# Kernel optimization log

Measured on AMD Instinct MI355X. Metric: run time of the kernel, lower is better.

The kernel has to match this reference:

```python
import jax, jax.numpy as jnp
import numpy as np

SIGMA_P = 0.01  # sigma_p from __init__
T = 2_000_000   # number of time samples / PMD steps


def _pauli():
    # Pauli spin matrices used by Czegledi (2016) rotation model
    return jnp.array([[[1, 0], [0, -1]],
                      [[0, 1], [1, 0]],
                      [[0, -1j], [1j, 0]]], dtype=jnp.complex64)


def setup_inputs() -> dict:
    key = jax.random.key(0)
    k1, k2, k3, k4 = jax.random.split(key, 4)
    signal_re = jax.random.normal(k1, (T, 2), dtype=jnp.float32)
    signal_im = jax.random.normal(k2, (T, 2), dtype=jnp.float32)
    alphas = jax.random.normal(k3, (T, 3), dtype=jnp.float32)  # raw N(0,1); scaled by SIGMA_P inside reference
    # initial Jones matrix J_k1 built from a random unit 4-vector (as in __init__)
    g = jax.random.normal(k4, (4,), dtype=jnp.float32)
    a0 = g / jnp.linalg.norm(g)
    theta0 = jnp.arccos(a0[0])
    alpha = a0[1:] / jnp.sin(theta0) * theta0
    theta = jnp.linalg.norm(alpha)
    a = (alpha / theta).astype(jnp.complex64)
    J0 = (jnp.eye(2, dtype=jnp.complex64) * jnp.cos(theta)
          - 1j * jnp.einsum('a,aij->ij', a, _pauli()) * jnp.sin(theta))
    return {"signal_re": signal_re, "signal_im": signal_im, "alphas": alphas,
            "J0_re": jnp.real(J0), "J0_im": jnp.imag(J0)}


def reference(signal_re, signal_im, alphas, J0_re, J0_im):
    pauli = _pauli()
    al = alphas * SIGMA_P                      # [T,3] per-step rotation vectors
    thetas = jnp.linalg.norm(al, axis=1)       # [T]
    a = (al / thetas[:, None]).astype(jnp.complex64)   # [T,3] unit axes
    eye = jnp.eye(2, dtype=jnp.complex64)
    # per-step incremental Jones matrices: J_delta[k] = I*cos(th) - i*(a.sigma)*sin(th)
    J_delta = (eye[None, :, :] * jnp.cos(thetas)[:, None, None]
               - 1j * jnp.einsum('ka,aij->kij', a, pauli) * jnp.sin(thetas)[:, None, None])  # [T,2,2]
    # cumulative left-product: chain[k] = J_delta[k] @ ... @ J_delta[0]
    chain = jax.lax.associative_scan(lambda x, y: jnp.matmul(y, x), J_delta)  # [T,2,2]
    J0 = (J0_re + 1j * J0_im).astype(jnp.complex64)
    J_k = jnp.einsum('kij,jl->kil', chain, J0)  # [T,2,2] time-varying Jones matrices
    signal = (signal_re + 1j * signal_im).astype(jnp.complex64)  # [T,2]
    return jnp.einsum('kij,kj->ki', J_k, signal)  # [T,2] complex64
```

## Files before the change

kernel.cpp:

```cpp
#include <hip/hip_runtime.h>
#include <hip/hip_bf16.h>

#define BLK 256
#define CH 8

__device__ __forceinline__ float4 qmul(const float4 A, const float4 B) {
    return make_float4(
        A.x*B.x - A.y*B.y - A.z*B.z - A.w*B.w,
        A.x*B.y + B.x*A.y + A.z*B.w - A.w*B.z,
        A.x*B.z + B.x*A.z + A.w*B.y - A.y*B.w,
        A.x*B.w + B.x*A.w + A.y*B.z - A.z*B.y);
}

__device__ __forceinline__ float4 qid() { return make_float4(1.f, 0.f, 0.f, 0.f); }

__device__ __forceinline__ float4 qnorm(const float4 q) {
    float n = rsqrtf(q.x*q.x + q.y*q.y + q.z*q.z + q.w*q.w);
    return make_float4(q.x*n, q.y*n, q.z*n, q.w*n);
}

__device__ __forceinline__ float4 dquat(float a0, float a1, float a2) {
    float x = a0 * 0.01f, y = a1 * 0.01f, z = a2 * 0.01f;
    float t2 = x*x + y*y + z*z;
    float c = 1.f - t2 * (0.5f - t2 * (1.f / 24.f));
    float f = 1.f - t2 * ((1.f / 6.f) - t2 * (1.f / 120.f));
    return make_float4(c, f*x, f*y, f*z);
}

__device__ __forceinline__ float4 qapply(const float4 m, float s0r, float s1r,
                                         float s0i, float s1i) {
    float w = m.x, v1 = m.y, v2 = m.z, v3 = m.w;
    return make_float4(
        w*s0r + v1*s0i - v3*s1r + v2*s1i,
        w*s0i - v1*s0r - v2*s1r - v3*s1i,
        v3*s0r + v2*s0i + w*s1r - v1*s1i,
        v3*s0i - v2*s0r + w*s1i + v1*s1r);
}

__device__ __forceinline__ float4 shfl_up4(const float4 v, int s) {
    return make_float4(__shfl_up(v.x, s), __shfl_up(v.y, s),
                       __shfl_up(v.z, s), __shfl_up(v.w, s));
}
__device__ __forceinline__ float4 shfl_down4(const float4 v, int s) {
    return make_float4(__shfl_down(v.x, s), __shfl_down(v.y, s),
                       __shfl_down(v.z, s), __shfl_down(v.w, s));
}

__device__ __forceinline__ float4 wave_prod_desc(float4 c) {
    #pragma unroll
    for (int s = 1; s < 64; s <<= 1) {
        float4 u = shfl_down4(c, s);
        c = qmul(u, c);
    }
    return c;
}

__device__ __forceinline__ float4 wave_scan_incl(float4 v, int lane) {
    #pragma unroll
    for (int s = 1; s < 64; s <<= 1) {
        float4 u = shfl_up4(v, s);
        if (lane >= s) v = qmul(v, u);
    }
    return v;
}

__device__ __forceinline__ float4 chunk_quats(const float* __restrict__ al,
                                              long long t, long long T,
                                              long long nchunk, float4* d, bool& full) {
    float4 q = qid();
    full = false;
    if (t >= nchunk) {
        #pragma unroll
        for (int j = 0; j < CH; ++j) d[j] = qid();
        return q;
    }
    if ((t + 1) * CH <= T) {
        full = true;
        const float4* ap = reinterpret_cast<const float4*>(al) + (size_t)t * 6;
        float4 v0 = ap[0], v1 = ap[1], v2 = ap[2];
        float4 v3 = ap[3], v4 = ap[4], v5 = ap[5];
        d[0] = dquat(v0.x, v0.y, v0.z);
        d[1] = dquat(v0.w, v1.x, v1.y);
        d[2] = dquat(v1.z, v1.w, v2.x);
        d[3] = dquat(v2.y, v2.z, v2.w);
        d[4] = dquat(v3.x, v3.y, v3.z);
        d[5] = dquat(v3.w, v4.x, v4.y);
        d[6] = dquat(v4.z, v4.w, v5.x);
        d[7] = dquat(v5.y, v5.z, v5.w);
    } else {
        #pragma unroll
        for (int j = 0; j < CH; ++j) {
            long long k = t * CH + j;
            d[j] = (k < T) ? dquat(al[k*3], al[k*3+1], al[k*3+2]) : qid();
        }
    }
    #pragma unroll
    for (int j = 0; j < CH; ++j) q = qmul(d[j], q);
    return qnorm(q);
}

__device__ __forceinline__ float4 chunk_prod(const float* __restrict__ al,
                                             long long t, long long T,
                                             long long nchunk) {
    float4 d[CH];
    bool full;
    return chunk_quats(al, t, T, nchunk, d, full);
}

__device__ __forceinline__ void apply_and_store(
    const float4* d, float4 run, bool full, long long t, long long T,
    const float* __restrict__ sre, const float* __restrict__ sim,
    float* __restrict__ outf) {
    if (full) {
        const float4* rp = reinterpret_cast<const float4*>(sre) + (size_t)t * 4;
        const float4* ip = reinterpret_cast<const float4*>(sim) + (size_t)t * 4;
        float4* op = reinterpret_cast<float4*>(outf) + (size_t)t * 4;
        float4 r0 = rp[0], r1 = rp[1], r2 = rp[2], r3 = rp[3];
        float4 i0 = ip[0], i1 = ip[1], i2 = ip[2], i3 = ip[3];
        float4 p0, p1;
        run = qmul(d[0], run); p0 = qapply(run, r0.x, r0.y, i0.x, i0.y);
        run = qmul(d[1], run); p1 = qapply(run, r0.z, r0.w, i0.z, i0.w);
        op[0] = make_float4(p0.x, p0.z, p1.x, p1.z);
        run = qmul(d[2], run); p0 = qapply(run, r1.x, r1.y, i1.x, i1.y);
        run = qmul(d[3], run); p1 = qapply(run, r1.z, r1.w, i1.z, i1.w);
        op[1] = make_float4(p0.x, p0.z, p1.x, p1.z);
        run = qmul(d[4], run); p0 = qapply(run, r2.x, r2.y, i2.x, i2.y);
        run = qmul(d[5], run); p1 = qapply(run, r2.z, r2.w, i2.z, i2.w);
        op[2] = make_float4(p0.x, p0.z, p1.x, p1.z);
        run = qmul(d[6], run); p0 = qapply(run, r3.x, r3.y, i3.x, i3.y);
        run = qmul(d[7], run); p1 = qapply(run, r3.z, r3.w, i3.z, i3.w);
        op[3] = make_float4(p0.x, p0.z, p1.x, p1.z);
    } else {
        float2* op2 = reinterpret_cast<float2*>(outf);
        #pragma unroll
        for (int j = 0; j < CH; ++j) {
            long long k = t * CH + j;
            if (k < T) {
                run = qmul(d[j], run);
                float4 p = qapply(run, sre[k*2], sre[k*2+1], sim[k*2], sim[k*2+1]);
                op2[k] = make_float2(p.x, p.z);
            }
        }
    }
}

__global__ void __launch_bounds__(BLK) pmd_k1(
    const float* __restrict__ al, float4* __restrict__ A,
    long long T, long long nchunk) {
    __shared__ float4 sW[BLK / 64];
    const int tid = threadIdx.x, lane = tid & 63, wid = tid >> 6;
    const long long t = (long long)blockIdx.x * BLK + tid;
    float4 q = chunk_prod(al, t, T, nchunk);
    float4 wp = wave_prod_desc(q);
    if (lane == 0) sW[wid] = wp;
    __syncthreads();
    if (tid == 0) {
        float4 a = qmul(sW[1], sW[0]);
        a = qmul(sW[2], a);
        a = qmul(sW[3], a);
        A[blockIdx.x] = qnorm(a);
    }
}

template<int EPT>
__global__ void __launch_bounds__(BLK) pmd_k2(
    const float4* __restrict__ A, float4* __restrict__ EB,
    const float* __restrict__ j0re, const float* __restrict__ j0im, int nblk) {
    __shared__ float4 sW[BLK / 64];
    const int tid = threadIdx.x, lane = tid & 63, wid = tid >> 6;
    const int t0 = tid * EPT;
    float4 excl[EPT];
    float4 run = qid();
    #pragma unroll
    for (int e = 0; e < EPT; ++e) {
        excl[e] = run;
        if (t0 + e < nblk) run = qmul(A[t0 + e], run);
    }
    float4 v = wave_scan_incl(run, lane);
    if (lane == 63) sW[wid] = v;
    __syncthreads();
    float4 P = qid();
    for (int w = 0; w < wid; ++w) P = qmul(sW[w], P);
    float4 vprev = shfl_up4(v, 1);
    float4 texcl = (lane == 0) ? P : qmul(vprev, P);
    float4 q0 = make_float4(j0re[0], -j0im[0], -j0im[1], -j0re[1]);
    float4 base = qmul(texcl, q0);
    #pragma unroll
    for (int e = 0; e < EPT; ++e) {
        if (t0 + e < nblk) EB[t0 + e] = qnorm(qmul(excl[e], base));
    }
}

__global__ void __launch_bounds__(BLK) pmd_k3(
    const float* __restrict__ al, const float* __restrict__ sre,
    const float* __restrict__ sim, const float4* __restrict__ EB,
    float* __restrict__ outf, long long T, long long nchunk) {
    __shared__ float4 sW[BLK / 64];
    const int tid = threadIdx.x, lane = tid & 63, wid = tid >> 6;
    const int b = blockIdx.x;
    const long long t = (long long)b * BLK + tid;

    float4 d[CH];
    bool full;
    float4 q = chunk_quats(al, t, T, nchunk, d, full);
    float4 v = wave_scan_incl(q, lane);
    if (lane == 63) sW[wid] = v;
    __syncthreads();
    float4 P = qid();
    for (int w = 0; w < wid; ++w) P = qmul(sW[w], P);
    float4 vprev = shfl_up4(v, 1);
    float4 Xv = (lane == 0) ? P : qmul(vprev, P);
    float4 run = qmul(Xv, EB[b]);
    if (t < nchunk)
        apply_and_store(d, run, full, t, T, sre, sim, outf);
}

__global__ void __launch_bounds__(BLK) pmd_mono(
    const float* __restrict__ al, const float* __restrict__ sre,
    const float* __restrict__ sim, const float* __restrict__ j0re,
    const float* __restrict__ j0im, float* __restrict__ outf, long long T) {
    __shared__ float4 sW[BLK / 64];
    __shared__ float4 sbase;
    const int tid = threadIdx.x, lane = tid & 63, wid = tid >> 6;
    if (tid == 0)
        sbase = make_float4(j0re[0], -j0im[0], -j0im[1], -j0re[1]);
    __syncthreads();
    const long long nchunk = (T + CH - 1) / CH;
    for (long long c0 = 0; c0 < nchunk; c0 += BLK) {
        const long long t = c0 + tid;
        float4 d[CH];
        bool full;
        float4 q = chunk_quats(al, t, T, nchunk, d, full);
        float4 v = wave_scan_incl(q, lane);
        if (lane == 63) sW[wid] = v;
        __syncthreads();
        float4 P = qid();
        for (int w = 0; w < wid; ++w) P = qmul(sW[w], P);
        float4 vprev = shfl_up4(v, 1);
        float4 Xv = (lane == 0) ? P : qmul(vprev, P);
        float4 base = sbase;
        __syncthreads();
        if (tid == BLK - 1) sbase = qnorm(qmul(qmul(v, P), base));
        if (t < nchunk) {
            float4 run = qmul(Xv, base);
            apply_and_store(d, run, full, t, T, sre, sim, outf);
        }
        __syncthreads();
    }
}

extern "C" void kernel_launch(void* const* d_in, const int* in_sizes, int n_in,
                              void* d_out, int out_size, void* d_ws, size_t ws_size,
                              hipStream_t stream) {
    const float* sre  = (const float*)d_in[0];
    const float* sim  = (const float*)d_in[1];
    const float* al   = (const float*)d_in[2];
    const float* j0re = (const float*)d_in[3];
    const float* j0im = (const float*)d_in[4];
    float* outf = (float*)d_out;
    long long T = (long long)in_sizes[2] / 3;
    if (T <= 0) return;

    long long nchunk = (T + CH - 1) / CH;
    long long nblkLL = (nchunk + BLK - 1) / BLK;
    size_t need = (size_t)(2 * nblkLL) * sizeof(float4);

    if (ws_size >= need && nblkLL <= (long long)BLK * 16) {
        int nblk = (int)nblkLL;
        float4* A  = (float4*)d_ws;
        float4* EB = A + nblk;
        pmd_k1<<<nblk, BLK, 0, stream>>>(al, A, T, nchunk);
        if      (nblk <= BLK)      pmd_k2<1> <<<1, BLK, 0, stream>>>(A, EB, j0re, j0im, nblk);
        else if (nblk <= 2 * BLK)  pmd_k2<2> <<<1, BLK, 0, stream>>>(A, EB, j0re, j0im, nblk);
        else if (nblk <= 4 * BLK)  pmd_k2<4> <<<1, BLK, 0, stream>>>(A, EB, j0re, j0im, nblk);
        else if (nblk <= 8 * BLK)  pmd_k2<8> <<<1, BLK, 0, stream>>>(A, EB, j0re, j0im, nblk);
        else                       pmd_k2<16><<<1, BLK, 0, stream>>>(A, EB, j0re, j0im, nblk);
        pmd_k3<<<nblk, BLK, 0, stream>>>(al, sre, sim, EB, outf, T, nchunk);
    } else {
        pmd_mono<<<1, BLK, 0, stream>>>(al, sre, sim, j0re, j0im, outf, T);
    }
}
```

Baseline: 28.88 us.

## Fuse block-reduce and block-prefix kernels using last-block ticket pattern

Merges the per-block quaternion reduction and the single-block prefix scan into one kernel. Each block increments an atomic ticket, and the last block to finish loads all block products into shared memory and computes the exclusive prefixes. The intent is to remove one kernel launch and its dependency gap. In exchange it adds a memset before the launch and a 16KB shared array per block, which may reduce occupancy, and the tail work runs on a single block.

```diff
diff --git a/kernel.cpp b/kernel.cpp
--- a/kernel.cpp
+++ b/kernel.cpp
@@ -3,6 +3,7 @@
 
 #define BLK 256
 #define CH 8
+#define MAXBLK 1024
 
 __device__ __forceinline__ float4 qmul(const float4 A, const float4 B) {
     return make_float4(
@@ -144,12 +145,16 @@
     }
 }
 
-__global__ void __launch_bounds__(BLK) pmd_k1(
-    const float* __restrict__ al, float4* __restrict__ A,
-    long long T, long long nchunk) {
-    __shared__ float4 sW[BLK / 64];
+__global__ void __launch_bounds__(BLK) pmd_k12(
+    const float* __restrict__ al, float4* __restrict__ A, float4* __restrict__ EB,
+    const float* __restrict__ j0re, const float* __restrict__ j0im,
+    unsigned* __restrict__ ticket, long long T, long long nchunk, int nblk) {
+    __shared__ float4 sW[BLK / 64];
+    __shared__ float4 sA[MAXBLK];
+    __shared__ int sIsLast;
     const int tid = threadIdx.x, lane = tid & 63, wid = tid >> 6;
     const long long t = (long long)blockIdx.x * BLK + tid;
+
     float4 q = chunk_prod(al, t, T, nchunk);
     float4 wp = wave_prod_desc(q);
     if (lane == 0) sW[wid] = wp;
@@ -159,23 +164,22 @@
         a = qmul(sW[2], a);
         a = qmul(sW[3], a);
         A[blockIdx.x] = qnorm(a);
-    }
-}
-
-template<int EPT>
-__global__ void __launch_bounds__(BLK) pmd_k2(
-    const float4* __restrict__ A, float4* __restrict__ EB,
-    const float* __restrict__ j0re, const float* __restrict__ j0im, int nblk) {
-    __shared__ float4 sW[BLK / 64];
-    const int tid = threadIdx.x, lane = tid & 63, wid = tid >> 6;
-    const int t0 = tid * EPT;
-    float4 excl[EPT];
+        __threadfence();
+        unsigned old = atomicAdd(ticket, 1u);
+        sIsLast = (old == (unsigned)(nblk - 1));
+    }
+    __syncthreads();
+    if (!sIsLast) return;
+
+    __threadfence();
+    for (int i = tid; i < nblk; i += BLK) sA[i] = A[i];
+    __syncthreads();
+
+    const int ept = (nblk + BLK - 1) / BLK;
+    const int t0 = tid * ept;
     float4 run = qid();
-    #pragma unroll
-    for (int e = 0; e < EPT; ++e) {
-        excl[e] = run;
-        if (t0 + e < nblk) run = qmul(A[t0 + e], run);
-    }
+    for (int e = 0; e < ept; ++e)
+        if (t0 + e < nblk) run = qmul(sA[t0 + e], run);
     float4 v = wave_scan_incl(run, lane);
     if (lane == 63) sW[wid] = v;
     __syncthreads();
@@ -185,9 +189,12 @@
     float4 texcl = (lane == 0) ? P : qmul(vprev, P);
     float4 q0 = make_float4(j0re[0], -j0im[0], -j0im[1], -j0re[1]);
     float4 base = qmul(texcl, q0);
-    #pragma unroll
-    for (int e = 0; e < EPT; ++e) {
-        if (t0 + e < nblk) EB[t0 + e] = qnorm(qmul(excl[e], base));
+    float4 excl = qid();
+    for (int e = 0; e < ept; ++e) {
+        if (t0 + e < nblk) {
+            EB[t0 + e] = qnorm(qmul(excl, base));
+            excl = qmul(sA[t0 + e], excl);
+        }
     }
 }
 
@@ -213,6 +220,53 @@
     float4 run = qmul(Xv, EB[b]);
     if (t < nchunk)
         apply_and_store(d, run, full, t, T, sre, sim, outf);
+}
+
+__global__ void __launch_bounds__(BLK) pmd_k1(
+    const float* __restrict__ al, float4* __restrict__ A,
+    long long T, long long nchunk) {
+    __shared__ float4 sW[BLK / 64];
+    const int tid = threadIdx.x, lane = tid & 63, wid = tid >> 6;
+    const long long t = (long long)blockIdx.x * BLK + tid;
+    float4 q = chunk_prod(al, t, T, nchunk);
+    float4 wp = wave_prod_desc(q);
+    if (lane == 0) sW[wid] = wp;
+    __syncthreads();
+    if (tid == 0) {
+        float4 a = qmul(sW[1], sW[0]);
+        a = qmul(sW[2], a);
+        a = qmul(sW[3], a);
+        A[blockIdx.x] = qnorm(a);
+    }
+}
+
+template<int EPT>
+__global__ void __launch_bounds__(BLK) pmd_k2(
+    const float4* __restrict__ A, float4* __restrict__ EB,
+    const float* __restrict__ j0re, const float* __restrict__ j0im, int nblk) {
+    __shared__ float4 sW[BLK / 64];
+    const int tid = threadIdx.x, lane = tid & 63, wid = tid >> 6;
+    const int t0 = tid * EPT;
+    float4 excl[EPT];
+    float4 run = qid();
+    #pragma unroll
+    for (int e = 0; e < EPT; ++e) {
+        excl[e] = run;
+        if (t0 + e < nblk) run = qmul(A[t0 + e], run);
+    }
+    float4 v = wave_scan_incl(run, lane);
+    if (lane == 63) sW[wid] = v;
+    __syncthreads();
+    float4 P = qid();
+    for (int w = 0; w < wid; ++w) P = qmul(sW[w], P);
+    float4 vprev = shfl_up4(v, 1);
+    float4 texcl = (lane == 0) ? P : qmul(vprev, P);
+    float4 q0 = make_float4(j0re[0], -j0im[0], -j0im[1], -j0re[1]);
+    float4 base = qmul(texcl, q0);
+    #pragma unroll
+    for (int e = 0; e < EPT; ++e) {
+        if (t0 + e < nblk) EB[t0 + e] = qnorm(qmul(excl[e], base));
+    }
 }
 
 __global__ void __launch_bounds__(BLK) pmd_mono(
@@ -263,18 +317,23 @@
 
     long long nchunk = (T + CH - 1) / CH;
     long long nblkLL = (nchunk + BLK - 1) / BLK;
-    size_t need = (size_t)(2 * nblkLL) * sizeof(float4);
+    size_t need = (size_t)(2 * nblkLL) * sizeof(float4) + 4;
 
     if (ws_size >= need && nblkLL <= (long long)BLK * 16) {
         int nblk = (int)nblkLL;
         float4* A  = (float4*)d_ws;
         float4* EB = A + nblk;
-        pmd_k1<<<nblk, BLK, 0, stream>>>(al, A, T, nchunk);
-        if      (nblk <= BLK)      pmd_k2<1> <<<1, BLK, 0, stream>>>(A, EB, j0re, j0im, nblk);
-        else if (nblk <= 2 * BLK)  pmd_k2<2> <<<1, BLK, 0, stream>>>(A, EB, j0re, j0im, nblk);
-        else if (nblk <= 4 * BLK)  pmd_k2<4> <<<1, BLK, 0, stream>>>(A, EB, j0re, j0im, nblk);
-        else if (nblk <= 8 * BLK)  pmd_k2<8> <<<1, BLK, 0, stream>>>(A, EB, j0re, j0im, nblk);
-        else                       pmd_k2<16><<<1, BLK, 0, stream>>>(A, EB, j0re, j0im, nblk);
+        unsigned* ticket = (unsigned*)(EB + nblk);
+        if (nblk <= MAXBLK) {
+            hipMemsetAsync(ticket, 0, sizeof(unsigned), stream);
+            pmd_k12<<<nblk, BLK, 0, stream>>>(al, A, EB, j0re, j0im, ticket,
+                                              T, nchunk, nblk);
+        } else {
+            pmd_k1<<<nblk, BLK, 0, stream>>>(al, A, T, nchunk);
+            if      (nblk <= 4 * BLK)  pmd_k2<4> <<<1, BLK, 0, stream>>>(A, EB, j0re, j0im, nblk);
+            else if (nblk <= 8 * BLK)  pmd_k2<8> <<<1, BLK, 0, stream>>>(A, EB, j0re, j0im, nblk);
+            else                       pmd_k2<16><<<1, BLK, 0, stream>>>(A, EB, j0re, j0im, nblk);
+        }
         pmd_k3<<<nblk, BLK, 0, stream>>>(al, sre, sim, EB, outf, T, nchunk);
     } else {
         pmd_mono<<<1, BLK, 0, stream>>>(al, sre, sim, j0re, j0im, outf, T);
```

Measured after the change: 52.09 us. 80.4% more time.

## Drop middle scan kernel; compute block prefixes via superblock aggregates in consumer

Applied to the files above, without the earlier changes.

Replaces the three-kernel reduce/scan/apply pipeline with two kernels. The first kernel computes per-block quaternion products plus a product per superblock of four blocks. The apply kernel has its first wave reduce all earlier superblock aggregates and then the within-superblock block products to form its exclusive prefix. This removes one kernel launch and the single-block serial scan, but every block now redundantly reads and reduces up to ~1000 superblock aggregates, and the first kernel has fewer, longer-running blocks.

```diff
diff --git a/kernel.cpp b/kernel.cpp
--- a/kernel.cpp
+++ b/kernel.cpp
@@ -3,6 +3,7 @@
 
 #define BLK 256
 #define CH 8
+#define SUPER 4
 
 __device__ __forceinline__ float4 qmul(const float4 A, const float4 B) {
     return make_float4(
@@ -144,6 +145,88 @@
     }
 }
 
+__global__ void __launch_bounds__(BLK) pmd_k1h(
+    const float* __restrict__ al, float4* __restrict__ A, float4* __restrict__ A2,
+    long long T, long long nchunk) {
+    __shared__ float4 sW[SUPER][BLK / 64];
+    const int tid = threadIdx.x, lane = tid & 63, wid = tid >> 6;
+    const int sb = blockIdx.x;
+    #pragma unroll
+    for (int j = 0; j < SUPER; ++j) {
+        long long t = ((long long)sb * SUPER + j) * BLK + tid;
+        float4 q = chunk_prod(al, t, T, nchunk);
+        float4 wp = wave_prod_desc(q);
+        if (lane == 0) sW[j][wid] = wp;
+    }
+    __syncthreads();
+    if (tid == 0) {
+        float4 acc = qid();
+        #pragma unroll
+        for (int j = 0; j < SUPER; ++j) {
+            float4 af = qmul(sW[j][1], sW[j][0]);
+            af = qmul(sW[j][2], af);
+            af = qmul(sW[j][3], af);
+            af = qnorm(af);
+            A[sb * SUPER + j] = af;
+            acc = qmul(af, acc);
+        }
+        A2[sb] = qnorm(acc);
+    }
+}
+
+__global__ void __launch_bounds__(BLK) pmd_k3h(
+    const float* __restrict__ al, const float* __restrict__ sre,
+    const float* __restrict__ sim, const float4* __restrict__ A,
+    const float4* __restrict__ A2, const float* __restrict__ j0re,
+    const float* __restrict__ j0im, float* __restrict__ outf,
+    long long T, long long nchunk) {
+    __shared__ float4 sW[BLK / 64];
+    __shared__ float4 sexcl;
+    const int tid = threadIdx.x, lane = tid & 63, wid = tid >> 6;
+    const int b = blockIdx.x;
+    const long long t = (long long)b * BLK + tid;
+
+    float4 d[CH];
+    bool full;
+    float4 q = chunk_quats(al, t, T, nchunk, d, full);
+    float4 v = wave_scan_incl(q, lane);
+    if (lane == 63) sW[wid] = v;
+
+    if (tid < 64) {
+        const int s = b / SUPER, r = b % SUPER;
+        float4 sp = qid();
+        if (s > 0) {
+            int top = s - 1;
+            int base = (top >> 6) << 6;
+            for (;;) {
+                int j = base + lane;
+                float4 c = (j <= top) ? A2[j] : qid();
+                float4 wp = wave_prod_desc(c);
+                sp = qmul(sp, wp);
+                if (base == 0) break;
+                top = base - 1;
+                base -= 64;
+            }
+        }
+        if (lane == 0) {
+            float4 fine = qid();
+            for (int i = 0; i < r; ++i) fine = qmul(A[s * SUPER + i], fine);
+            float4 tot = qmul(fine, sp);
+            float4 q0 = make_float4(j0re[0], -j0im[0], -j0im[1], -j0re[1]);
+            sexcl = qnorm(qmul(tot, q0));
+        }
+    }
+    __syncthreads();
+
+    float4 P = qid();
+    for (int w = 0; w < wid; ++w) P = qmul(sW[w], P);
+    float4 vprev = shfl_up4(v, 1);
+    float4 Xv = (lane == 0) ? P : qmul(vprev, P);
+    float4 run = qmul(Xv, sexcl);
+    if (t < nchunk)
+        apply_and_store(d, run, full, t, T, sre, sim, outf);
+}
+
 __global__ void __launch_bounds__(BLK) pmd_k1(
     const float* __restrict__ al, float4* __restrict__ A,
     long long T, long long nchunk) {
@@ -199,7 +282,6 @@
     const int tid = threadIdx.x, lane = tid & 63, wid = tid >> 6;
     const int b = blockIdx.x;
     const long long t = (long long)b * BLK + tid;
-
     float4 d[CH];
     bool full;
     float4 q = chunk_quats(al, t, T, nchunk, d, full);
@@ -263,9 +345,18 @@
 
     long long nchunk = (T + CH - 1) / CH;
     long long nblkLL = (nchunk + BLK - 1) / BLK;
-    size_t need = (size_t)(2 * nblkLL) * sizeof(float4);
-
-    if (ws_size >= need && nblkLL <= (long long)BLK * 16) {
+    long long nsupLL = (nblkLL + SUPER - 1) / SUPER;
+    size_t need_h = (size_t)(nsupLL * SUPER + nsupLL) * sizeof(float4);
+    size_t need_f = (size_t)(2 * nblkLL) * sizeof(float4);
+
+    if (ws_size >= need_h && nsupLL <= 1024) {
+        int nblk = (int)nblkLL, nsup = (int)nsupLL;
+        float4* A  = (float4*)d_ws;
+        float4* A2 = A + (size_t)nsup * SUPER;
+        pmd_k1h<<<nsup, BLK, 0, stream>>>(al, A, A2, T, nchunk);
+        pmd_k3h<<<nblk, BLK, 0, stream>>>(al, sre, sim, A, A2, j0re, j0im,
+                                          outf, T, nchunk);
+    } else if (ws_size >= need_f && nblkLL <= (long long)BLK * 16) {
         int nblk = (int)nblkLL;
         float4* A  = (float4*)d_ws;
         float4* EB = A + nblk;
```

Measured after the change: 30.82 us. +6.7%, slower.

## Drop single-block block-scan kernel; each block reduces its own prefix of block aggregates

Applied to the files above, without the earlier changes.

Removes the middle single-workgroup scan kernel that turned per-block quaternion aggregates into exclusive prefixes. Each block of the final kernel now reduces all preceding block aggregates itself, split across its four waves with wave-level products, then combines them with J0. This saves one kernel launch and a serialized single-block step, at the cost of redundant prefix work that grows with block index. With about 977 blocks, each wave reads at most roughly four 64-entry segments.

```diff
diff --git a/kernel.cpp b/kernel.cpp
--- a/kernel.cpp
+++ b/kernel.cpp
@@ -162,43 +162,31 @@
     }
 }
 
-template<int EPT>
-__global__ void __launch_bounds__(BLK) pmd_k2(
-    const float4* __restrict__ A, float4* __restrict__ EB,
-    const float* __restrict__ j0re, const float* __restrict__ j0im, int nblk) {
-    __shared__ float4 sW[BLK / 64];
-    const int tid = threadIdx.x, lane = tid & 63, wid = tid >> 6;
-    const int t0 = tid * EPT;
-    float4 excl[EPT];
-    float4 run = qid();
-    #pragma unroll
-    for (int e = 0; e < EPT; ++e) {
-        excl[e] = run;
-        if (t0 + e < nblk) run = qmul(A[t0 + e], run);
-    }
-    float4 v = wave_scan_incl(run, lane);
-    if (lane == 63) sW[wid] = v;
-    __syncthreads();
-    float4 P = qid();
-    for (int w = 0; w < wid; ++w) P = qmul(sW[w], P);
-    float4 vprev = shfl_up4(v, 1);
-    float4 texcl = (lane == 0) ? P : qmul(vprev, P);
-    float4 q0 = make_float4(j0re[0], -j0im[0], -j0im[1], -j0re[1]);
-    float4 base = qmul(texcl, q0);
-    #pragma unroll
-    for (int e = 0; e < EPT; ++e) {
-        if (t0 + e < nblk) EB[t0 + e] = qnorm(qmul(excl[e], base));
-    }
-}
-
-__global__ void __launch_bounds__(BLK) pmd_k3(
+__global__ void __launch_bounds__(BLK) pmd_k3s(
     const float* __restrict__ al, const float* __restrict__ sre,
-    const float* __restrict__ sim, const float4* __restrict__ EB,
+    const float* __restrict__ sim, const float4* __restrict__ A,
+    const float* __restrict__ j0re, const float* __restrict__ j0im,
     float* __restrict__ outf, long long T, long long nchunk) {
     __shared__ float4 sW[BLK / 64];
+    __shared__ float4 sSp[BLK / 64];
     const int tid = threadIdx.x, lane = tid & 63, wid = tid >> 6;
     const int b = blockIdx.x;
     const long long t = (long long)b * BLK + tid;
+
+    float4 part = qid();
+    if (b > 0) {
+        const int S = ((b - 1) >> 6) + 1;
+        const int R = (S + 3) >> 2;
+        const int s_lo = wid * R;
+        const int s_hi = min(S, s_lo + R);
+        for (int s = s_lo; s < s_hi; ++s) {
+            int idx = (s << 6) + lane;
+            float4 c = (idx <= b - 1) ? A[idx] : qid();
+            float4 sp = wave_prod_desc(c);
+            part = qmul(sp, part);
+        }
+    }
+    if (lane == 0) sSp[wid] = part;
 
     float4 d[CH];
     bool full;
@@ -206,11 +194,16 @@
     float4 v = wave_scan_incl(q, lane);
     if (lane == 63) sW[wid] = v;
     __syncthreads();
+
+    float4 sp = qmul(qmul(sSp[3], sSp[2]), qmul(sSp[1], sSp[0]));
+    float4 q0 = make_float4(j0re[0], -j0im[0], -j0im[1], -j0re[1]);
+    float4 sexcl = qnorm(qmul(sp, q0));
+
     float4 P = qid();
     for (int w = 0; w < wid; ++w) P = qmul(sW[w], P);
     float4 vprev = shfl_up4(v, 1);
     float4 Xv = (lane == 0) ? P : qmul(vprev, P);
-    float4 run = qmul(Xv, EB[b]);
+    float4 run = qmul(Xv, sexcl);
     if (t < nchunk)
         apply_and_store(d, run, full, t, T, sre, sim, outf);
 }
@@ -263,19 +256,14 @@
 
     long long nchunk = (T + CH - 1) / CH;
     long long nblkLL = (nchunk + BLK - 1) / BLK;
-    size_t need = (size_t)(2 * nblkLL) * sizeof(float4);
-
-    if (ws_size >= need && nblkLL <= (long long)BLK * 16) {
+    size_t need = (size_t)nblkLL * sizeof(float4);
+
+    if (ws_size >= need && nblkLL <= 0x7fffffff) {
         int nblk = (int)nblkLL;
-        float4* A  = (float4*)d_ws;
-        float4* EB = A + nblk;
+        float4* A = (float4*)d_ws;
         pmd_k1<<<nblk, BLK, 0, stream>>>(al, A, T, nchunk);
-        if      (nblk <= BLK)      pmd_k2<1> <<<1, BLK, 0, stream>>>(A, EB, j0re, j0im, nblk);
-        else if (nblk <= 2 * BLK)  pmd_k2<2> <<<1, BLK, 0, stream>>>(A, EB, j0re, j0im, nblk);
-        else if (nblk <= 4 * BLK)  pmd_k2<4> <<<1, BLK, 0, stream>>>(A, EB, j0re, j0im, nblk);
-        else if (nblk <= 8 * BLK)  pmd_k2<8> <<<1, BLK, 0, stream>>>(A, EB, j0re, j0im, nblk);
-        else                       pmd_k2<16><<<1, BLK, 0, stream>>>(A, EB, j0re, j0im, nblk);
-        pmd_k3<<<nblk, BLK, 0, stream>>>(al, sre, sim, EB, outf, T, nchunk);
+        pmd_k3s<<<nblk, BLK, 0, stream>>>(al, sre, sim, A, j0re, j0im,
+                                          outf, T, nchunk);
     } else {
         pmd_mono<<<1, BLK, 0, stream>>>(al, sre, sim, j0re, j0im, outf, T);
     }
```

Result: slower. 30.96 us (+7.2%).
